# Performance work log

Hardware: AMD Instinct MI355X
Metric: run time of the kernel (lower is better)

Reference implementation:

```python
import jax, jax.numpy as jnp
import numpy as np

DIM, NHEADS = 1024, 16
HD = DIM // NHEADS
ROPE_BASE = 10000.0


def rope_cos_sin(seq_len, hd):
    inv_freq = 1.0 / (ROPE_BASE ** (jnp.arange(0, hd, 2, dtype=jnp.float32) / hd))
    t = jnp.arange(seq_len, dtype=jnp.float32)
    freqs = jnp.outer(t, inv_freq)              # [N, hd/2]
    emb = jnp.concatenate([freqs, freqs], -1)   # [N, hd]
    return jnp.cos(emb), jnp.sin(emb)


def rotate_half(x):
    h = x.shape[-1] // 2
    return jnp.concatenate([-x[..., h:], x[..., :h]], -1)


def setup_inputs() -> dict:
    key = jax.random.key(0)
    ks = jax.random.split(key, 5)
    B, N = 1, 2048
    x = jax.random.normal(ks[0], (B, N, DIM), jnp.float32)
    wq = jax.random.normal(ks[1], (DIM, DIM), jnp.float32) * 0.02
    wk = jax.random.normal(ks[2], (DIM, DIM), jnp.float32) * 0.02
    wv = jax.random.normal(ks[3], (DIM, DIM), jnp.float32) * 0.02
    wp = jax.random.normal(ks[4], (DIM, DIM), jnp.float32) * 0.02
    return {"x": x, "wq": wq, "wk": wk, "wv": wv, "wp": wp}


def reference(x, wq, wk, wv, wp):
    B, N, D = x.shape
    H, hd = NHEADS, HD
    # nn.Linear: y = x @ W.T (weights stored [out, in])
    q = (x @ wq.T).reshape(B, N, H, hd)
    k = (x @ wk.T).reshape(B, N, H, hd)
    v = (x @ wv.T).reshape(B, N, H, hd)
    cos, sin = rope_cos_sin(N, hd)
    cos = cos[None, :, None, :]
    sin = sin[None, :, None, :]
    q = q * cos + rotate_half(q) * sin
    k = k * cos + rotate_half(k) * sin
    # SDPA (no mask, non-causal, eval -> no dropout)
    scale = 1.0 / jnp.sqrt(jnp.float32(hd))
    logits = jnp.einsum("bqhd,bkhd->bhqk", q, k) * scale
    attn = jax.nn.softmax(logits, axis=-1)
    out = jnp.einsum("bhqk,bkhd->bqhd", attn, v).reshape(B, N, D)
    return out @ wp.T
```

## Files before the change

kernel.cpp:

```cpp
#include <hip/hip_runtime.h>

typedef short s16x8 __attribute__((ext_vector_type(8)));
typedef float f32x4 __attribute__((ext_vector_type(4)));
typedef float f32x16 __attribute__((ext_vector_type(16)));

__device__ __forceinline__ unsigned short f2bf(float f) {
    unsigned int u = __float_as_uint(f);
    u += 0x7fff + ((u >> 16) & 1);
    return (unsigned short)(u >> 16);
}
__device__ __forceinline__ float bf2f(unsigned short h) {
    return __uint_as_float(((unsigned int)h) << 16);
}
__device__ __forceinline__ f32x4 mfma16(s16x8 a, s16x8 b, f32x4 c) {
    return __builtin_amdgcn_mfma_f32_16x16x32_bf16(a, b, c, 0, 0, 0);
}
__device__ __forceinline__ f32x16 mfma32(s16x8 a, s16x8 b, f32x16 c) {
    return __builtin_amdgcn_mfma_f32_32x32x16_bf16(a, b, c, 0, 0, 0);
}
__device__ __forceinline__ void async16(const void* g, void* l) {
    __builtin_amdgcn_global_load_lds(
        (const __attribute__((address_space(1))) void*)g,
        (__attribute__((address_space(3))) void*)l, 16, 0, 0);
}

__global__ __launch_bounds__(256) void convert_all(
    const float* __restrict__ x,  const float* __restrict__ wq,
    const float* __restrict__ wk, const float* __restrict__ wv,
    const float* __restrict__ wp,
    unsigned short* __restrict__ xb, unsigned short* __restrict__ wqkvb,
    unsigned short* __restrict__ wpb)
{
    const size_t XN = 2048u * 1024u, WN = 1024u * 1024u;
    size_t e = ((size_t)blockIdx.x * 256 + threadIdx.x) * 4;
    const float* s; unsigned short* d;
    if (e < XN)                { s = x  + e;               d = xb    + e; }
    else if (e < XN + WN)      { s = wq + (e - XN);        d = wqkvb + (e - XN); }
    else if (e < XN + 2 * WN)  { s = wk + (e - XN - WN);   d = wqkvb + (e - XN); }
    else if (e < XN + 3 * WN)  { s = wv + (e - XN - 2*WN); d = wqkvb + (e - XN); }
    else                       { s = wp + (e - XN - 3*WN); d = wpb   + (e - XN - 3*WN); }
    float4 v = *(const float4*)s;
    ushort4 o;
    o.x = f2bf(v.x); o.y = f2bf(v.y); o.z = f2bf(v.z); o.w = f2bf(v.w);
    *(ushort4*)d = o;
}

template<int BM, int BN, int C32>
__global__ __launch_bounds__(256) void gemm_mfma(
    const unsigned short* __restrict__ A,
    const unsigned short* __restrict__ B,
    void* __restrict__ C, int Ntot, int kLen, size_t cSlice)
{
    constexpr int MT = BM / 32, NT = BN / 32;
    __shared__ unsigned short As[BM * 64];
    __shared__ unsigned short Bs[BN * 64];

    const int tid  = threadIdx.x;
    const int wave = tid >> 6, lane = tid & 63;
    const int l16  = lane & 15, quad = lane >> 4;
    const int m0   = blockIdx.y * BM, n0 = blockIdx.x * BN;
    const int kB   = blockIdx.z * kLen;
    const int wm   = (wave & 1) * (BM / 2), wn = (wave >> 1) * (BN / 2);

    const int srow8 = lane >> 3;
    const int scol  = (lane & 7) * 8;

    f32x4 acc[MT][NT] = {};

    for (int k0 = kB; k0 < kB + kLen; k0 += 64) {
        #pragma unroll
        for (int i = 0; i < BM / 32; i++) {
            int j = wave * (BM / 32) + i;
            async16(A + (size_t)(m0 + j * 8 + srow8) * 1024 + k0 + scol, &As[j * 512]);
        }
        #pragma unroll
        for (int i = 0; i < BN / 32; i++) {
            int j = wave * (BN / 32) + i;
            async16(B + (size_t)(n0 + j * 8 + srow8) * 1024 + k0 + scol, &Bs[j * 512]);
        }
        __syncthreads();

        #pragma unroll
        for (int ks = 0; ks < 2; ks++) {
            s16x8 af[MT], bfr[NT];
            #pragma unroll
            for (int mt = 0; mt < MT; mt++)
                af[mt] = *(const s16x8*)&As[(wm + mt * 16 + l16) * 64 + ks * 32 + quad * 8];
            #pragma unroll
            for (int nt = 0; nt < NT; nt++)
                bfr[nt] = *(const s16x8*)&Bs[(wn + nt * 16 + l16) * 64 + ks * 32 + quad * 8];
            #pragma unroll
            for (int mt = 0; mt < MT; mt++)
                #pragma unroll
                for (int nt = 0; nt < NT; nt++)
                    acc[mt][nt] = mfma16(af[mt], bfr[nt], acc[mt][nt]);
        }
        __syncthreads();
    }

    #pragma unroll
    for (int mt = 0; mt < MT; mt++)
        #pragma unroll
        for (int nt = 0; nt < NT; nt++)
            #pragma unroll
            for (int r = 0; r < 4; r++) {
                int m = m0 + wm + mt * 16 + quad * 4 + r;
                int n = n0 + wn + nt * 16 + l16;
                size_t idx = (size_t)blockIdx.z * cSlice + (size_t)m * Ntot + n;
                if (C32) ((float*)C)[idx] = acc[mt][nt][r];
                else     ((unsigned short*)C)[idx] = f2bf(acc[mt][nt][r]);
            }
}

__global__ __launch_bounds__(256) void reduce_proj(
    const float* __restrict__ P, float* __restrict__ out)
{
    size_t e = ((size_t)blockIdx.x * 256 + threadIdx.x) * 4;
    float4 a = *(const float4*)(P + e);
    float4 b = *(const float4*)(P + (size_t)2048 * 1024 + e);
    float4 o;
    o.x = a.x + b.x; o.y = a.y + b.y; o.z = a.z + b.z; o.w = a.w + b.w;
    *(float4*)(out + e) = o;
}

__global__ __launch_bounds__(256) void rope_kernel(unsigned short* __restrict__ qkv)
{
    int idx = blockIdx.x * 256 + threadIdx.x;
    int i = idx & 31;
    int h = (idx >> 5) & 15;
    int n = idx >> 9;
    float ang = (float)n * exp2f((float)i * (-13.287712379549449f / 32.0f));
    float c, s;
    sincosf(ang, &c, &s);
    size_t base = (size_t)n * 3072 + h * 64 + i;
    float a0 = bf2f(qkv[base]), a1 = bf2f(qkv[base + 32]);
    qkv[base]      = f2bf(a0 * c + a1 * s);
    qkv[base + 32] = f2bf(a1 * c - a0 * s);
    float b0 = bf2f(qkv[base + 1024]), b1 = bf2f(qkv[base + 1056]);
    qkv[base + 1024] = f2bf(b0 * c + b1 * s);
    qkv[base + 1056] = f2bf(b1 * c - b0 * s);
}

__global__ __launch_bounds__(256, 4) void attn_part(
    const unsigned short* __restrict__ qkv,
    float* __restrict__ Opart, float* __restrict__ Lpart)
{
    const int h  = blockIdx.y;
    const int q0 = blockIdx.x * 128;
    const int ks = blockIdx.z;
    const int tid  = threadIdx.x;
    const int wave = tid >> 6, lane = tid & 63;
    const int l32  = lane & 31, half = lane >> 5;

    __shared__ unsigned short Ks[64][72];
    __shared__ unsigned short Vt[64][72];
    __shared__ unsigned short Ps[4][32][72];

    const unsigned short* qp = qkv + (size_t)(q0 + wave * 32 + l32) * 3072 + h * 64 + half * 8;
    s16x8 qb[4];
    #pragma unroll
    for (int c = 0; c < 4; c++)
        qb[c] = *(const s16x8*)(qp + c * 16);

    f32x16 o0 = {}, o1 = {};
    float lsum = 0.f;

    for (int t = 0; t < 8; t++) {
        const int kt = ks * 512 + t * 64;

        if (tid < 128) {
            int g  = tid & 15;
            int d0 = (tid >> 4) * 8;
            const unsigned short* gv = qkv + (size_t)(kt + 4 * g) * 3072 + 2048 + h * 64 + d0;
            unsigned short a0[8], a1[8], a2[8], a3[8];
            *(uint4*)a0 = *(const uint4*)gv;
            *(uint4*)a1 = *(const uint4*)(gv + 3072);
            *(uint4*)a2 = *(const uint4*)(gv + 6144);
            *(uint4*)a3 = *(const uint4*)(gv + 9216);
            #pragma unroll
            for (int d = 0; d < 8; d++) {
                ushort4 w;
                w.x = a0[d]; w.y = a1[d]; w.z = a2[d]; w.w = a3[d];
                *(ushort4*)&Vt[d0 + d][4 * g] = w;
            }
        } else {
            int u = tid - 128;
            int key = u & 63;
            int dh = (u >> 6) * 32;
            const unsigned short* gk = qkv + (size_t)(kt + key) * 3072 + 1024 + h * 64 + dh;
            const uint4* g4 = (const uint4*)gk;
            uint4 k0 = g4[0], k1 = g4[1], k2 = g4[2], k3 = g4[3];
            *(uint4*)&Ks[key][dh]      = k0;
            *(uint4*)&Ks[key][dh + 8]  = k1;
            *(uint4*)&Ks[key][dh + 16] = k2;
            *(uint4*)&Ks[key][dh + 24] = k3;
        }
        __syncthreads();

        #pragma unroll
        for (int g = 0; g < 2; g++) {
            f32x16 s = {};
            #pragma unroll
            for (int c = 0; c < 4; c++) {
                s16x8 ka = *(const s16x8*)&Ks[g * 32 + l32][c * 16 + half * 8];
                s = mfma32(ka, qb[c], s);
            }
            #pragma unroll
            for (int c = 0; c < 4; c++) {
                float e0 = __expf(s[4 * c + 0] * 0.125f);
                float e1 = __expf(s[4 * c + 1] * 0.125f);
                float e2 = __expf(s[4 * c + 2] * 0.125f);
                float e3 = __expf(s[4 * c + 3] * 0.125f);
                lsum += (e0 + e1) + (e2 + e3);
                ushort4 w;
                w.x = f2bf(e0); w.y = f2bf(e1); w.z = f2bf(e2); w.w = f2bf(e3);
                *(ushort4*)&Ps[wave][l32][g * 32 + c * 8 + half * 4] = w;
            }
        }

        #pragma unroll
        for (int c = 0; c < 4; c++) {
            s16x8 pa = *(const s16x8*)&Ps[wave][l32][c * 16 + half * 8];
            s16x8 v0 = *(const s16x8*)&Vt[l32][c * 16 + half * 8];
            s16x8 v1 = *(const s16x8*)&Vt[32 + l32][c * 16 + half * 8];
            o0 = mfma32(pa, v0, o0);
            o1 = mfma32(pa, v1, o1);
        }
        __syncthreads();
    }

    lsum += __shfl_xor(lsum, 32, 64);

    const int mq = q0 + wave * 32;
    float* opBase = Opart + (size_t)ks * 2048 * 1024;
    #pragma unroll
    for (int r = 0; r < 16; r++) {
        int qr = (r & 3) + 8 * (r >> 2) + 4 * half;
        float* op = opBase + (size_t)(mq + qr) * 1024 + h * 64;
        op[l32]      = o0[r];
        op[32 + l32] = o1[r];
    }
    if (half == 0)
        Lpart[((size_t)ks * 2048 + mq + l32) * 16 + h] = lsum;
}

__global__ __launch_bounds__(256) void combine(
    const float* __restrict__ Opart, const float* __restrict__ Lpart,
    unsigned short* __restrict__ ab)
{
    size_t e = ((size_t)blockIdx.x * 256 + threadIdx.x) * 4;
    int tok = (int)(e >> 10);
    int h = (int)((e & 1023) >> 6);
    float l = 0.f;
    #pragma unroll
    for (int s = 0; s < 4; s++)
        l += Lpart[((size_t)s * 2048 + tok) * 16 + h];
    float inv = 1.0f / l;
    float4 acc = *(const float4*)(Opart + e);
    #pragma unroll
    for (int s = 1; s < 4; s++) {
        float4 n = *(const float4*)(Opart + (size_t)s * 2048 * 1024 + e);
        acc.x += n.x; acc.y += n.y; acc.z += n.z; acc.w += n.w;
    }
    ushort4 w;
    w.x = f2bf(acc.x * inv);
    w.y = f2bf(acc.y * inv);
    w.z = f2bf(acc.z * inv);
    w.w = f2bf(acc.w * inv);
    *(ushort4*)(ab + e) = w;
}

extern "C" void kernel_launch(void* const* d_in, const int* in_sizes, int n_in,
                              void* d_out, int out_size, void* d_ws, size_t ws_size,
                              hipStream_t stream)
{
    const float* x  = (const float*)d_in[0];
    const float* wq = (const float*)d_in[1];
    const float* wk = (const float*)d_in[2];
    const float* wv = (const float*)d_in[3];
    const float* wp = (const float*)d_in[4];

    unsigned short* xb    = (unsigned short*)d_ws;
    unsigned short* wqkvb = xb    + 2u * 1024 * 1024;
    unsigned short* wpb   = wqkvb + 3u * 1024 * 1024;
    unsigned short* qkv   = wpb   + 1u * 1024 * 1024;
    unsigned short* ab    = qkv   + 2048u * 3072;
    float* Opart    = (float*)(ab + 2u * 1024 * 1024);
    float* Lpart    = Opart + 4u * 2048 * 1024;
    float* projPart = Lpart + 4u * 2048 * 16;

    convert_all<<<6144, 256, 0, stream>>>(x, wq, wk, wv, wp, xb, wqkvb, wpb);
    gemm_mfma<128, 128, 0><<<dim3(24, 16, 1), 256, 0, stream>>>(
        xb, wqkvb, qkv, 3072, 1024, 0);
    rope_kernel<<<(2048 * 512) / 256, 256, 0, stream>>>(qkv);
    attn_part<<<dim3(16, 16, 4), 256, 0, stream>>>(qkv, Opart, Lpart);
    combine<<<2048, 256, 0, stream>>>(Opart, Lpart, ab);
    gemm_mfma<64, 64, 1><<<dim3(16, 32, 2), 256, 0, stream>>>(
        ab, wpb, projPart, 1024, 512, (size_t)2048 * 1024);
    reduce_proj<<<2048, 256, 0, stream>>>(projPart, (float*)d_out);
}
```

Baseline: 163.1 us.

## Fuse RoPE into QKV GEMM, store bf16 partials, drop proj split-K

RoPE is now applied in the QKV GEMM epilogue. Each wave's 64-column slice is one head, so the rotation pairs are accumulator tiles nt and nt+2; this removes the separate rope kernel's read-modify-write pass over q and k. The QKV GEMM tile changes from 128x128 to 64x128, doubling the block count. Attention partial outputs are stored as bf16 instead of fp32, halving the Opart write and read traffic in combine, with some loss of precision in the unnormalized partial sums. The output projection drops split-K and writes fp32 directly to the output, which eliminates the reduce_proj kernel and the projPart buffer.

```diff
diff --git a/kernel.cpp b/kernel.cpp
--- a/kernel.cpp
+++ b/kernel.cpp
@@ -23,6 +23,8 @@
         (const __attribute__((address_space(1))) void*)g,
         (__attribute__((address_space(3))) void*)l, 16, 0, 0);
 }
+
+#define ROPE_C (-13.287712379549449f / 32.0f)
 
 __global__ __launch_bounds__(256) void convert_all(
     const float* __restrict__ x,  const float* __restrict__ wq,
@@ -45,11 +47,11 @@
     *(ushort4*)d = o;
 }
 
-template<int BM, int BN, int C32>
+template<int BM, int BN, int C32, int ROPE>
 __global__ __launch_bounds__(256) void gemm_mfma(
     const unsigned short* __restrict__ A,
     const unsigned short* __restrict__ B,
-    void* __restrict__ C, int Ntot, int kLen, size_t cSlice)
+    void* __restrict__ C, int Ntot)
 {
     constexpr int MT = BM / 32, NT = BN / 32;
     __shared__ unsigned short As[BM * 64];
@@ -59,7 +61,6 @@
     const int wave = tid >> 6, lane = tid & 63;
     const int l16  = lane & 15, quad = lane >> 4;
     const int m0   = blockIdx.y * BM, n0 = blockIdx.x * BN;
-    const int kB   = blockIdx.z * kLen;
     const int wm   = (wave & 1) * (BM / 2), wn = (wave >> 1) * (BN / 2);
 
     const int srow8 = lane >> 3;
@@ -67,7 +68,7 @@
 
     f32x4 acc[MT][NT] = {};
 
-    for (int k0 = kB; k0 < kB + kLen; k0 += 64) {
+    for (int k0 = 0; k0 < 1024; k0 += 64) {
         #pragma unroll
         for (int i = 0; i < BM / 32; i++) {
             int j = wave * (BM / 32) + i;
@@ -98,6 +99,27 @@
         __syncthreads();
     }
 
+    if constexpr (ROPE) {
+        if (n0 < 2048) {
+            #pragma unroll
+            for (int mt = 0; mt < MT; mt++)
+                #pragma unroll
+                for (int r = 0; r < 4; r++) {
+                    int m = m0 + wm + mt * 16 + quad * 4 + r;
+                    #pragma unroll
+                    for (int nt = 0; nt < 2; nt++) {
+                        int i = nt * 16 + l16;
+                        float ang = (float)m * exp2f((float)i * ROPE_C);
+                        float c, s;
+                        sincosf(ang, &c, &s);
+                        float e0 = acc[mt][nt][r], e1 = acc[mt][nt + 2][r];
+                        acc[mt][nt][r]     = e0 * c + e1 * s;
+                        acc[mt][nt + 2][r] = e1 * c - e0 * s;
+                    }
+                }
+        }
+    }
+
     #pragma unroll
     for (int mt = 0; mt < MT; mt++)
         #pragma unroll
@@ -106,44 +128,15 @@
             for (int r = 0; r < 4; r++) {
                 int m = m0 + wm + mt * 16 + quad * 4 + r;
                 int n = n0 + wn + nt * 16 + l16;
-                size_t idx = (size_t)blockIdx.z * cSlice + (size_t)m * Ntot + n;
+                size_t idx = (size_t)m * Ntot + n;
                 if (C32) ((float*)C)[idx] = acc[mt][nt][r];
                 else     ((unsigned short*)C)[idx] = f2bf(acc[mt][nt][r]);
             }
 }
 
-__global__ __launch_bounds__(256) void reduce_proj(
-    const float* __restrict__ P, float* __restrict__ out)
-{
-    size_t e = ((size_t)blockIdx.x * 256 + threadIdx.x) * 4;
-    float4 a = *(const float4*)(P + e);
-    float4 b = *(const float4*)(P + (size_t)2048 * 1024 + e);
-    float4 o;
-    o.x = a.x + b.x; o.y = a.y + b.y; o.z = a.z + b.z; o.w = a.w + b.w;
-    *(float4*)(out + e) = o;
-}
-
-__global__ __launch_bounds__(256) void rope_kernel(unsigned short* __restrict__ qkv)
-{
-    int idx = blockIdx.x * 256 + threadIdx.x;
-    int i = idx & 31;
-    int h = (idx >> 5) & 15;
-    int n = idx >> 9;
-    float ang = (float)n * exp2f((float)i * (-13.287712379549449f / 32.0f));
-    float c, s;
-    sincosf(ang, &c, &s);
-    size_t base = (size_t)n * 3072 + h * 64 + i;
-    float a0 = bf2f(qkv[base]), a1 = bf2f(qkv[base + 32]);
-    qkv[base]      = f2bf(a0 * c + a1 * s);
-    qkv[base + 32] = f2bf(a1 * c - a0 * s);
-    float b0 = bf2f(qkv[base + 1024]), b1 = bf2f(qkv[base + 1056]);
-    qkv[base + 1024] = f2bf(b0 * c + b1 * s);
-    qkv[base + 1056] = f2bf(b1 * c - b0 * s);
-}
-
 __global__ __launch_bounds__(256, 4) void attn_part(
     const unsigned short* __restrict__ qkv,
-    float* __restrict__ Opart, float* __restrict__ Lpart)
+    unsigned short* __restrict__ Opart, float* __restrict__ Lpart)
 {
     const int h  = blockIdx.y;
     const int q0 = blockIdx.x * 128;
@@ -232,20 +225,20 @@
     lsum += __shfl_xor(lsum, 32, 64);
 
     const int mq = q0 + wave * 32;
-    float* opBase = Opart + (size_t)ks * 2048 * 1024;
+    unsigned short* opBase = Opart + (size_t)ks * 2048 * 1024;
     #pragma unroll
     for (int r = 0; r < 16; r++) {
         int qr = (r & 3) + 8 * (r >> 2) + 4 * half;
-        float* op = opBase + (size_t)(mq + qr) * 1024 + h * 64;
-        op[l32]      = o0[r];
-        op[32 + l32] = o1[r];
+        unsigned short* op = opBase + (size_t)(mq + qr) * 1024 + h * 64;
+        op[l32]      = f2bf(o0[r]);
+        op[32 + l32] = f2bf(o1[r]);
     }
     if (half == 0)
         Lpart[((size_t)ks * 2048 + mq + l32) * 16 + h] = lsum;
 }
 
 __global__ __launch_bounds__(256) void combine(
-    const float* __restrict__ Opart, const float* __restrict__ Lpart,
+    const unsigned short* __restrict__ Opart, const float* __restrict__ Lpart,
     unsigned short* __restrict__ ab)
 {
     size_t e = ((size_t)blockIdx.x * 256 + threadIdx.x) * 4;
@@ -256,17 +249,17 @@
     for (int s = 0; s < 4; s++)
         l += Lpart[((size_t)s * 2048 + tok) * 16 + h];
     float inv = 1.0f / l;
-    float4 acc = *(const float4*)(Opart + e);
-    #pragma unroll
-    for (int s = 1; s < 4; s++) {
-        float4 n = *(const float4*)(Opart + (size_t)s * 2048 * 1024 + e);
-        acc.x += n.x; acc.y += n.y; acc.z += n.z; acc.w += n.w;
+    float a0 = 0.f, a1 = 0.f, a2 = 0.f, a3 = 0.f;
+    #pragma unroll
+    for (int s = 0; s < 4; s++) {
+        ushort4 n = *(const ushort4*)(Opart + (size_t)s * 2048 * 1024 + e);
+        a0 += bf2f(n.x); a1 += bf2f(n.y); a2 += bf2f(n.z); a3 += bf2f(n.w);
     }
     ushort4 w;
-    w.x = f2bf(acc.x * inv);
-    w.y = f2bf(acc.y * inv);
-    w.z = f2bf(acc.z * inv);
-    w.w = f2bf(acc.w * inv);
+    w.x = f2bf(a0 * inv);
+    w.y = f2bf(a1 * inv);
+    w.z = f2bf(a2 * inv);
+    w.w = f2bf(a3 * inv);
     *(ushort4*)(ab + e) = w;
 }
 
@@ -285,17 +278,14 @@
     unsigned short* wpb   = wqkvb + 3u * 1024 * 1024;
     unsigned short* qkv   = wpb   + 1u * 1024 * 1024;
     unsigned short* ab    = qkv   + 2048u * 3072;
-    float* Opart    = (float*)(ab + 2u * 1024 * 1024);
-    float* Lpart    = Opart + 4u * 2048 * 1024;
-    float* projPart = Lpart + 4u * 2048 * 16;
+    unsigned short* Opart = ab    + 2u * 1024 * 1024;
+    float* Lpart = (float*)(Opart + 4u * 2048 * 1024);
 
     convert_all<<<6144, 256, 0, stream>>>(x, wq, wk, wv, wp, xb, wqkvb, wpb);
-    gemm_mfma<128, 128, 0><<<dim3(24, 16, 1), 256, 0, stream>>>(
-        xb, wqkvb, qkv, 3072, 1024, 0);
-    rope_kernel<<<(2048 * 512) / 256, 256, 0, stream>>>(qkv);
+    gemm_mfma<64, 128, 0, 1><<<dim3(24, 32), 256, 0, stream>>>(
+        xb, wqkvb, qkv, 3072);
     attn_part<<<dim3(16, 16, 4), 256, 0, stream>>>(qkv, Opart, Lpart);
     combine<<<2048, 256, 0, stream>>>(Opart, Lpart, ab);
-    gemm_mfma<64, 64, 1><<<dim3(16, 32, 2), 256, 0, stream>>>(
-        ab, wpb, projPart, 1024, 512, (size_t)2048 * 1024);
-    reduce_proj<<<2048, 256, 0, stream>>>(projPart, (float*)d_out);
-}
+    gemm_mfma<64, 64, 1, 0><<<dim3(16, 32), 256, 0, stream>>>(
+        ab, wpb, d_out, 1024);
+}
```

Result: faster. 155.0 us (-5.0%).
